# Optimization experiments

Measured on AMD Instinct MI355X. Metric: run time of the kernel, lower is better.

Reference implementation:

```python
import jax, jax.numpy as jnp
import numpy as np

N_STATIONS = 100000
N_TIME = 365
N_NEIGHBORS = 5
SMOOTHING = 0.1


def setup_inputs() -> dict:
    key = jax.random.key(0)
    k = jax.random.split(key, 6)
    N, T, K = N_STATIONS, N_TIME, N_NEIGHBORS
    time_vector = jnp.arange(T, dtype=jnp.float32) / 365.25  # years
    constant_offset = jax.random.normal(k[0], (N,), jnp.float32) * 10.0
    linear_trend = jax.random.normal(k[1], (N,), jnp.float32) * 5.0  # mm/yr (ps00_rates buffer)
    seasonal_amplitudes = jax.random.uniform(k[2], (N, 4), jnp.float32) * 6.0
    seasonal_phases = jax.random.uniform(k[3], (N, 4), jnp.float32) * (2.0 * np.pi)
    neighbor_indices = jax.random.randint(k[4], (N, K), 0, N)
    w = jax.random.uniform(k[5], (N, K), jnp.float32) + 1e-3
    neighbor_weights = w / jnp.sum(w, axis=1, keepdims=True)  # row-normalized, like exp-dist weights
    periods = jnp.array([0.25, 0.5, 1.0, 2.0], dtype=jnp.float32)
    return {
        'time_vector': time_vector,
        'constant_offset': constant_offset,
        'linear_trend': linear_trend,
        'seasonal_amplitudes': seasonal_amplitudes,
        'seasonal_phases': seasonal_phases,
        'neighbor_weights': neighbor_weights,
        'periods': periods,
        'neighbor_indices': neighbor_indices,
    }


def _smooth(p, neighbor_indices, neighbor_weights):
    # p: [N, 4]; vectorized version of per-station loop: gather + weighted mean
    nb = p[neighbor_indices]                                   # [N, K, 4]
    avg = jnp.einsum('nkf,nk->nf', nb, neighbor_weights)       # [N, 4]
    return (1.0 - SMOOTHING) * p + SMOOTHING * avg


def reference(time_vector, constant_offset, linear_trend, seasonal_amplitudes,
              seasonal_phases, neighbor_weights, periods, neighbor_indices):
    amps = _smooth(seasonal_amplitudes, neighbor_indices, neighbor_weights)   # [N, 4]
    phs = _smooth(seasonal_phases, neighbor_indices, neighbor_weights)        # [N, 4]
    t = time_vector[None, :]                                                  # [1, T]
    signals = constant_offset[:, None] + linear_trend[:, None] * t           # [N, T]
    two_pi = jnp.float32(2.0 * np.pi)
    for f in range(4):  # fixed small set of seasonal periods
        freq = 1.0 / periods[f]
        signals = signals + amps[:, f:f + 1] * jnp.sin(two_pi * freq * t + phs[:, f:f + 1])
    return signals
```

## Files before the change

### kernel.cpp

```cpp
#include <hip/hip_runtime.h>
#include <math.h>

typedef float f32x2 __attribute__((ext_vector_type(2)));
typedef float f32x4 __attribute__((ext_vector_type(4)));

#define TWO_PI 6.283185307179586f
#define SMOOTH 0.1f
#define SPW 8
#define WAVES 4
#define BLOCK 256
#define SPB (SPW * WAVES)
#define NPAIR 3

__device__ __forceinline__ f32x2 sp2(float x) { f32x2 r; r.x = x; r.y = x; return r; }
__device__ __forceinline__ float rlane(float v, int l) {
    return __uint_as_float((unsigned)__builtin_amdgcn_readlane((int)__float_as_uint(v), l));
}

template<int TT>
__global__ __launch_bounds__(BLOCK) void fused_v14(
    const float* __restrict__ time_vector,
    const float* __restrict__ constant_offset,
    const float* __restrict__ linear_trend,
    const float* __restrict__ amps,
    const float* __restrict__ phs,
    const float* __restrict__ wgt,
    const float* __restrict__ periods,
    const int*   __restrict__ nbidx,
    float* __restrict__ out,
    int N, int T_rt, int K)
{
    const int T = (TT > 0) ? TT : T_rt;
    extern __shared__ float slab[];

    const int tid    = threadIdx.x;
    const int wave   = tid >> 6;
    const int lane   = tid & 63;
    const int bbase  = blockIdx.x * SPB;
    const int wbase  = bbase + wave * SPW;

    if (bbase >= N) return;
    int bsend = N - bbase; if (bsend > SPB) bsend = SPB;

    int sid = wbase + (lane & (SPW - 1));
    if (sid >= N) sid = N - 1;

    float4 a = reinterpret_cast<const float4*>(amps)[sid];
    float4 p = reinterpret_cast<const float4*>(phs)[sid];

    int   nb[5]; float w[5];
    __builtin_memcpy(nb, nbidx + (size_t)sid * K, 5 * sizeof(int));
    __builtin_memcpy(w,  wgt   + (size_t)sid * K, 5 * sizeof(float));

    float av0 = 0.f, av1 = 0.f, av2 = 0.f, av3 = 0.f;
    float pv0 = 0.f, pv1 = 0.f, pv2 = 0.f, pv3 = 0.f;
    #pragma unroll
    for (int k = 0; k < 5; ++k) {
        float4 na = reinterpret_cast<const float4*>(amps)[nb[k]];
        float4 np = reinterpret_cast<const float4*>(phs)[nb[k]];
        av0 += w[k] * na.x; av1 += w[k] * na.y; av2 += w[k] * na.z; av3 += w[k] * na.w;
        pv0 += w[k] * np.x; pv1 += w[k] * np.y; pv2 += w[k] * np.z; pv3 += w[k] * np.w;
    }
    float sa0 = (1.0f - SMOOTH) * a.x + SMOOTH * av0;
    float sa1 = (1.0f - SMOOTH) * a.y + SMOOTH * av1;
    float sa2 = (1.0f - SMOOTH) * a.z + SMOOTH * av2;
    float sa3 = (1.0f - SMOOTH) * a.w + SMOOTH * av3;
    float sp0 = (1.0f - SMOOTH) * p.x + SMOOTH * pv0;
    float sp1 = (1.0f - SMOOTH) * p.y + SMOOTH * pv1;
    float sp2v = (1.0f - SMOOTH) * p.z + SMOOTH * pv2;
    float sp3 = (1.0f - SMOOTH) * p.w + SMOOTH * pv3;

    float cc = constant_offset[sid];
    float cm = linear_trend[sid];
    float cA0 = sa0 * __cosf(sp0),  cB0 = sa0 * __sinf(sp0);
    float cA1 = sa1 * __cosf(sp1),  cB1 = sa1 * __sinf(sp1);
    float cA2 = sa2 * __cosf(sp2v), cB2 = sa2 * __sinf(sp2v);
    float cA3 = sa3 * __cosf(sp3),  cB3 = sa3 * __sinf(sp3);

    const float w0 = TWO_PI / periods[0];
    const float w1 = TWO_PI / periods[1];
    const float w2 = TWO_PI / periods[2];
    const float w3 = TWO_PI / periods[3];

    f32x2 tv[NPAIR];
    f32x2 bs[NPAIR][4], bc[NPAIR][4];
    bool full[NPAIR], any[NPAIR];
    const int t0 = 2 * lane;

    #pragma unroll
    for (int q = 0; q < NPAIR; ++q) {
        const int t = t0 + 128 * q;
        const bool v0 = (t < T), v1 = (t + 1 < T);
        any[q] = v0; full[q] = v1;
        float ta = v0 ? time_vector[t]     : 0.f;
        float tb = v1 ? time_vector[t + 1] : 0.f;
        f32x2 tvp; tvp.x = ta; tvp.y = tb;
        tv[q] = tvp;
        #pragma unroll
        for (int f = 0; f < 4; ++f) {
            const float wf = (f == 0) ? w0 : (f == 1) ? w1 : (f == 2) ? w2 : w3;
            f32x2 s, c;
            s.x = __sinf(wf * ta); s.y = __sinf(wf * tb);
            c.x = __cosf(wf * ta); c.y = __cosf(wf * tb);
            bs[q][f] = s; bc[q][f] = c;
        }
    }

    if (bsend == SPB) {
        float* wrows = slab + (size_t)(wave * SPW) * T;

        #pragma unroll
        for (int j = 0; j < SPW; ++j) {
            float sc  = rlane(cc,  j), sm  = rlane(cm,  j);
            float sA0 = rlane(cA0, j), sB0 = rlane(cB0, j);
            float sA1 = rlane(cA1, j), sB1 = rlane(cB1, j);
            float sA2 = rlane(cA2, j), sB2 = rlane(cB2, j);
            float sA3 = rlane(cA3, j), sB3 = rlane(cB3, j);
            float* lrow = wrows + j * T;

            #pragma unroll
            for (int q = 0; q < NPAIR; ++q) {
                f32x2 sig = sp2(sc) + sp2(sm) * tv[q];
                sig += sp2(sA0) * bs[q][0] + sp2(sB0) * bc[q][0];
                sig += sp2(sA1) * bs[q][1] + sp2(sB1) * bc[q][1];
                sig += sp2(sA2) * bs[q][2] + sp2(sB2) * bc[q][2];
                sig += sp2(sA3) * bs[q][3] + sp2(sB3) * bc[q][3];
                const int t = t0 + 128 * q;
                if (full[q]) { lrow[t] = sig.x; lrow[t + 1] = sig.y; }
                else if (any[q]) { lrow[t] = sig.x; }
            }
        }

        __syncthreads();

        const f32x4* lsrc = reinterpret_cast<const f32x4*>(slab);
        f32x4* gdst = reinterpret_cast<f32x4*>(out + (size_t)bbase * T);

        if (TT == 365) {
            f32x4 v0_ = lsrc[tid];          f32x4 v1_ = lsrc[tid + 256];
            f32x4 v2_ = lsrc[tid + 512];    f32x4 v3_ = lsrc[tid + 768];
            f32x4 v4_ = lsrc[tid + 1024];   f32x4 v5_ = lsrc[tid + 1280];
            f32x4 v6_ = lsrc[tid + 1536];   f32x4 v7_ = lsrc[tid + 1792];
            f32x4 v8_ = lsrc[tid + 2048];   f32x4 v9_ = lsrc[tid + 2304];
            f32x4 va_ = lsrc[tid + 2560];
            const bool extra = (tid < 104);
            f32x4 vb_;
            if (extra) vb_ = lsrc[tid + 2816];

            __builtin_nontemporal_store(v0_, gdst + tid);
            __builtin_nontemporal_store(v1_, gdst + tid + 256);
            __builtin_nontemporal_store(v2_, gdst + tid + 512);
            __builtin_nontemporal_store(v3_, gdst + tid + 768);
            __builtin_nontemporal_store(v4_, gdst + tid + 1024);
            __builtin_nontemporal_store(v5_, gdst + tid + 1280);
            __builtin_nontemporal_store(v6_, gdst + tid + 1536);
            __builtin_nontemporal_store(v7_, gdst + tid + 1792);
            __builtin_nontemporal_store(v8_, gdst + tid + 2048);
            __builtin_nontemporal_store(v9_, gdst + tid + 2304);
            __builtin_nontemporal_store(va_, gdst + tid + 2560);
            if (extra) __builtin_nontemporal_store(vb_, gdst + tid + 2816);
        } else {
            const int nch = (SPB * T) >> 2;
            for (int i = tid; i < nch; i += BLOCK) {
                f32x4 v = lsrc[i];
                __builtin_nontemporal_store(v, gdst + i);
            }
        }
    } else {
        int send = N - wbase; if (send > SPW) send = SPW;
        if (send <= 0) return;
        float* obase = out + (size_t)wbase * T;
        for (int j = 0; j < send; ++j) {
            float sc  = rlane(cc,  j), sm  = rlane(cm,  j);
            float sA0 = rlane(cA0, j), sB0 = rlane(cB0, j);
            float sA1 = rlane(cA1, j), sB1 = rlane(cB1, j);
            float sA2 = rlane(cA2, j), sB2 = rlane(cB2, j);
            float sA3 = rlane(cA3, j), sB3 = rlane(cB3, j);
            float* orow = obase + (size_t)j * T;
            #pragma unroll
            for (int q = 0; q < NPAIR; ++q) {
                f32x2 sig = sp2(sc) + sp2(sm) * tv[q];
                sig += sp2(sA0) * bs[q][0] + sp2(sB0) * bc[q][0];
                sig += sp2(sA1) * bs[q][1] + sp2(sB1) * bc[q][1];
                sig += sp2(sA2) * bs[q][2] + sp2(sB2) * bc[q][2];
                sig += sp2(sA3) * bs[q][3] + sp2(sB3) * bc[q][3];
                const int t = t0 + 128 * q;
                if (full[q]) { orow[t] = sig.x; orow[t + 1] = sig.y; }
                else if (any[q]) { orow[t] = sig.x; }
            }
        }
    }
}

extern "C" void kernel_launch(void* const* d_in, const int* in_sizes, int n_in,
                              void* d_out, int out_size, void* d_ws, size_t ws_size,
                              hipStream_t stream)
{
    const float* time_vector     = (const float*)d_in[0];
    const float* constant_offset = (const float*)d_in[1];
    const float* linear_trend    = (const float*)d_in[2];
    const float* amps            = (const float*)d_in[3];
    const float* phs             = (const float*)d_in[4];
    const float* wgt             = (const float*)d_in[5];
    const float* periods         = (const float*)d_in[6];
    const int*   nbidx           = (const int*)d_in[7];

    int T = in_sizes[0];
    int N = in_sizes[1];
    int K = in_sizes[5] / N;
    float* out = (float*)d_out;

    int grid = (N + SPB - 1) / SPB;
    size_t shmem = (size_t)SPB * T * sizeof(float);
    if (T == 365) {
        fused_v14<365><<<grid, BLOCK, shmem, stream>>>(
            time_vector, constant_offset, linear_trend, amps, phs, wgt,
            periods, nbidx, out, N, T, K);
    } else {
        fused_v14<0><<<grid, BLOCK, shmem, stream>>>(
            time_vector, constant_offset, linear_trend, amps, phs, wgt,
            periods, nbidx, out, N, T, K);
    }
}
```

Measured before the change: 35.77 us.

## Process four 32-station slabs per block, reusing sin/cos basis and LDS

Each block now handles four consecutive 32-station slabs instead of one. Lanes are split into four groups of eight so that all 32 stations' coefficients for a wave are gathered and smoothed in one pass. The per-thread sin/cos time basis is then reused across the slabs, and a single LDS buffer is recycled with a lightweight lgkmcnt+s_barrier between the compute and store phases. This cuts the grid to a quarter and amortizes the transcendental setup, at the cost of serializing the slabs inside a block and adding two barriers per slab.

```diff
diff --git a/kernel.cpp b/kernel.cpp
--- a/kernel.cpp
+++ b/kernel.cpp
@@ -9,16 +9,20 @@
 #define SPW 8
 #define WAVES 4
 #define BLOCK 256
-#define SPB (SPW * WAVES)
+#define SPB 32
+#define SLABS 4
 #define NPAIR 3
 
 __device__ __forceinline__ f32x2 sp2(float x) { f32x2 r; r.x = x; r.y = x; return r; }
 __device__ __forceinline__ float rlane(float v, int l) {
     return __uint_as_float((unsigned)__builtin_amdgcn_readlane((int)__float_as_uint(v), l));
 }
+__device__ __forceinline__ void barrier_lgkm() {
+    asm volatile("s_waitcnt lgkmcnt(0)\ns_barrier" ::: "memory");
+}
 
 template<int TT>
-__global__ __launch_bounds__(BLOCK) void fused_v14(
+__global__ __launch_bounds__(BLOCK) void fused_v16(
     const float* __restrict__ time_vector,
     const float* __restrict__ constant_offset,
     const float* __restrict__ linear_trend,
@@ -28,21 +32,20 @@
     const float* __restrict__ periods,
     const int*   __restrict__ nbidx,
     float* __restrict__ out,
-    int N, int T_rt, int K)
+    int N, int T_rt, int K, int nslab)
 {
     const int T = (TT > 0) ? TT : T_rt;
     extern __shared__ float slab[];
 
-    const int tid    = threadIdx.x;
-    const int wave   = tid >> 6;
-    const int lane   = tid & 63;
-    const int bbase  = blockIdx.x * SPB;
-    const int wbase  = bbase + wave * SPW;
-
-    if (bbase >= N) return;
-    int bsend = N - bbase; if (bsend > SPB) bsend = SPB;
-
-    int sid = wbase + (lane & (SPW - 1));
+    const int tid   = threadIdx.x;
+    const int wave  = tid >> 6;
+    const int lane  = tid & 63;
+    const int slab0 = blockIdx.x * SLABS;
+    if (slab0 >= nslab) return;
+
+    const int sgrp = (lane >> 3) & (SLABS - 1);
+    const int jrow = lane & 7;
+    int sid = (slab0 + sgrp) * SPB + wave * SPW + jrow;
     if (sid >= N) sid = N - 1;
 
     float4 a = reinterpret_cast<const float4*>(amps)[sid];
@@ -106,87 +109,100 @@
         }
     }
 
-    if (bsend == SPB) {
-        float* wrows = slab + (size_t)(wave * SPW) * T;
-
-        #pragma unroll
-        for (int j = 0; j < SPW; ++j) {
-            float sc  = rlane(cc,  j), sm  = rlane(cm,  j);
-            float sA0 = rlane(cA0, j), sB0 = rlane(cB0, j);
-            float sA1 = rlane(cA1, j), sB1 = rlane(cB1, j);
-            float sA2 = rlane(cA2, j), sB2 = rlane(cB2, j);
-            float sA3 = rlane(cA3, j), sB3 = rlane(cB3, j);
-            float* lrow = wrows + j * T;
-
+    float* wrows = slab + (size_t)(wave * SPW) * T;
+    const f32x4* lsrc = reinterpret_cast<const f32x4*>(slab);
+
+    #pragma unroll
+    for (int s = 0; s < SLABS; ++s) {
+        const int si = slab0 + s;
+        if (si >= nslab) break;
+        const int bbase = si * SPB;
+        const bool fullslab = (bbase + SPB <= N);
+
+        if (fullslab) {
             #pragma unroll
-            for (int q = 0; q < NPAIR; ++q) {
-                f32x2 sig = sp2(sc) + sp2(sm) * tv[q];
-                sig += sp2(sA0) * bs[q][0] + sp2(sB0) * bc[q][0];
-                sig += sp2(sA1) * bs[q][1] + sp2(sB1) * bc[q][1];
-                sig += sp2(sA2) * bs[q][2] + sp2(sB2) * bc[q][2];
-                sig += sp2(sA3) * bs[q][3] + sp2(sB3) * bc[q][3];
-                const int t = t0 + 128 * q;
-                if (full[q]) { lrow[t] = sig.x; lrow[t + 1] = sig.y; }
-                else if (any[q]) { lrow[t] = sig.x; }
+            for (int j = 0; j < SPW; ++j) {
+                const int src = (s << 3) | j;
+                float sc  = rlane(cc,  src), sm  = rlane(cm,  src);
+                float sA0 = rlane(cA0, src), sB0 = rlane(cB0, src);
+                float sA1 = rlane(cA1, src), sB1 = rlane(cB1, src);
+                float sA2 = rlane(cA2, src), sB2 = rlane(cB2, src);
+                float sA3 = rlane(cA3, src), sB3 = rlane(cB3, src);
+                float* lrow = wrows + j * T;
+
+                #pragma unroll
+                for (int q = 0; q < NPAIR; ++q) {
+                    f32x2 sig = sp2(sc) + sp2(sm) * tv[q];
+                    sig += sp2(sA0) * bs[q][0] + sp2(sB0) * bc[q][0];
+                    sig += sp2(sA1) * bs[q][1] + sp2(sB1) * bc[q][1];
+                    sig += sp2(sA2) * bs[q][2] + sp2(sB2) * bc[q][2];
+                    sig += sp2(sA3) * bs[q][3] + sp2(sB3) * bc[q][3];
+                    const int t = t0 + 128 * q;
+                    if (full[q]) { lrow[t] = sig.x; lrow[t + 1] = sig.y; }
+                    else if (any[q]) { lrow[t] = sig.x; }
+                }
             }
-        }
-
-        __syncthreads();
-
-        const f32x4* lsrc = reinterpret_cast<const f32x4*>(slab);
-        f32x4* gdst = reinterpret_cast<f32x4*>(out + (size_t)bbase * T);
-
-        if (TT == 365) {
-            f32x4 v0_ = lsrc[tid];          f32x4 v1_ = lsrc[tid + 256];
-            f32x4 v2_ = lsrc[tid + 512];    f32x4 v3_ = lsrc[tid + 768];
-            f32x4 v4_ = lsrc[tid + 1024];   f32x4 v5_ = lsrc[tid + 1280];
-            f32x4 v6_ = lsrc[tid + 1536];   f32x4 v7_ = lsrc[tid + 1792];
-            f32x4 v8_ = lsrc[tid + 2048];   f32x4 v9_ = lsrc[tid + 2304];
-            f32x4 va_ = lsrc[tid + 2560];
-            const bool extra = (tid < 104);
-            f32x4 vb_;
-            if (extra) vb_ = lsrc[tid + 2816];
-
-            __builtin_nontemporal_store(v0_, gdst + tid);
-            __builtin_nontemporal_store(v1_, gdst + tid + 256);
-            __builtin_nontemporal_store(v2_, gdst + tid + 512);
-            __builtin_nontemporal_store(v3_, gdst + tid + 768);
-            __builtin_nontemporal_store(v4_, gdst + tid + 1024);
-            __builtin_nontemporal_store(v5_, gdst + tid + 1280);
-            __builtin_nontemporal_store(v6_, gdst + tid + 1536);
-            __builtin_nontemporal_store(v7_, gdst + tid + 1792);
-            __builtin_nontemporal_store(v8_, gdst + tid + 2048);
-            __builtin_nontemporal_store(v9_, gdst + tid + 2304);
-            __builtin_nontemporal_store(va_, gdst + tid + 2560);
-            if (extra) __builtin_nontemporal_store(vb_, gdst + tid + 2816);
+
+            barrier_lgkm();
+
+            f32x4* gdst = reinterpret_cast<f32x4*>(out + (size_t)bbase * T);
+            if (TT == 365) {
+                f32x4 v0_ = lsrc[tid];          f32x4 v1_ = lsrc[tid + 256];
+                f32x4 v2_ = lsrc[tid + 512];    f32x4 v3_ = lsrc[tid + 768];
+                f32x4 v4_ = lsrc[tid + 1024];   f32x4 v5_ = lsrc[tid + 1280];
+                f32x4 v6_ = lsrc[tid + 1536];   f32x4 v7_ = lsrc[tid + 1792];
+                f32x4 v8_ = lsrc[tid + 2048];   f32x4 v9_ = lsrc[tid + 2304];
+                f32x4 va_ = lsrc[tid + 2560];
+                const bool extra = (tid < 104);
+                f32x4 vb_;
+                if (extra) vb_ = lsrc[tid + 2816];
+
+                __builtin_nontemporal_store(v0_, gdst + tid);
+                __builtin_nontemporal_store(v1_, gdst + tid + 256);
+                __builtin_nontemporal_store(v2_, gdst + tid + 512);
+                __builtin_nontemporal_store(v3_, gdst + tid + 768);
+                __builtin_nontemporal_store(v4_, gdst + tid + 1024);
+                __builtin_nontemporal_store(v5_, gdst + tid + 1280);
+                __builtin_nontemporal_store(v6_, gdst + tid + 1536);
+                __builtin_nontemporal_store(v7_, gdst + tid + 1792);
+                __builtin_nontemporal_store(v8_, gdst + tid + 2048);
+                __builtin_nontemporal_store(v9_, gdst + tid + 2304);
+                __builtin_nontemporal_store(va_, gdst + tid + 2560);
+                if (extra) __builtin_nontemporal_store(vb_, gdst + tid + 2816);
+            } else {
+                const int nch = (SPB * T) >> 2;
+                for (int i = tid; i < nch; i += BLOCK) {
+                    f32x4 v = lsrc[i];
+                    __builtin_nontemporal_store(v, gdst + i);
+                }
+            }
+
+            barrier_lgkm();
         } else {
-            const int nch = (SPB * T) >> 2;
-            for (int i = tid; i < nch; i += BLOCK) {
-                f32x4 v = lsrc[i];
-                __builtin_nontemporal_store(v, gdst + i);
-            }
-        }
-    } else {
-        int send = N - wbase; if (send > SPW) send = SPW;
-        if (send <= 0) return;
-        float* obase = out + (size_t)wbase * T;
-        for (int j = 0; j < send; ++j) {
-            float sc  = rlane(cc,  j), sm  = rlane(cm,  j);
-            float sA0 = rlane(cA0, j), sB0 = rlane(cB0, j);
-            float sA1 = rlane(cA1, j), sB1 = rlane(cB1, j);
-            float sA2 = rlane(cA2, j), sB2 = rlane(cB2, j);
-            float sA3 = rlane(cA3, j), sB3 = rlane(cB3, j);
-            float* orow = obase + (size_t)j * T;
-            #pragma unroll
-            for (int q = 0; q < NPAIR; ++q) {
-                f32x2 sig = sp2(sc) + sp2(sm) * tv[q];
-                sig += sp2(sA0) * bs[q][0] + sp2(sB0) * bc[q][0];
-                sig += sp2(sA1) * bs[q][1] + sp2(sB1) * bc[q][1];
-                sig += sp2(sA2) * bs[q][2] + sp2(sB2) * bc[q][2];
-                sig += sp2(sA3) * bs[q][3] + sp2(sB3) * bc[q][3];
-                const int t = t0 + 128 * q;
-                if (full[q]) { orow[t] = sig.x; orow[t + 1] = sig.y; }
-                else if (any[q]) { orow[t] = sig.x; }
+            int wfirst = bbase + wave * SPW;
+            int send = N - wfirst; if (send > SPW) send = SPW;
+            if (send > 0) {
+                float* obase = out + (size_t)wfirst * T;
+                for (int j = 0; j < send; ++j) {
+                    const int src = (s << 3) | j;
+                    float sc  = rlane(cc,  src), sm  = rlane(cm,  src);
+                    float sA0 = rlane(cA0, src), sB0 = rlane(cB0, src);
+                    float sA1 = rlane(cA1, src), sB1 = rlane(cB1, src);
+                    float sA2 = rlane(cA2, src), sB2 = rlane(cB2, src);
+                    float sA3 = rlane(cA3, src), sB3 = rlane(cB3, src);
+                    float* orow = obase + (size_t)j * T;
+                    #pragma unroll
+                    for (int q = 0; q < NPAIR; ++q) {
+                        f32x2 sig = sp2(sc) + sp2(sm) * tv[q];
+                        sig += sp2(sA0) * bs[q][0] + sp2(sB0) * bc[q][0];
+                        sig += sp2(sA1) * bs[q][1] + sp2(sB1) * bc[q][1];
+                        sig += sp2(sA2) * bs[q][2] + sp2(sB2) * bc[q][2];
+                        sig += sp2(sA3) * bs[q][3] + sp2(sB3) * bc[q][3];
+                        const int t = t0 + 128 * q;
+                        if (full[q]) { orow[t] = sig.x; orow[t + 1] = sig.y; }
+                        else if (any[q]) { orow[t] = sig.x; }
+                    }
+                }
             }
         }
     }
@@ -210,15 +226,17 @@
     int K = in_sizes[5] / N;
     float* out = (float*)d_out;
 
-    int grid = (N + SPB - 1) / SPB;
+    int nslab = (N + SPB - 1) / SPB;
+    int grid  = (nslab + SLABS - 1) / SLABS;
     size_t shmem = (size_t)SPB * T * sizeof(float);
+
     if (T == 365) {
-        fused_v14<365><<<grid, BLOCK, shmem, stream>>>(
+        fused_v16<365><<<grid, BLOCK, shmem, stream>>>(
             time_vector, constant_offset, linear_trend, amps, phs, wgt,
-            periods, nbidx, out, N, T, K);
+            periods, nbidx, out, N, T, K, nslab);
     } else {
-        fused_v14<0><<<grid, BLOCK, shmem, stream>>>(
+        fused_v16<0><<<grid, BLOCK, shmem, stream>>>(
             time_vector, constant_offset, linear_trend, amps, phs, wgt,
-            periods, nbidx, out, N, T, K);
-    }
-}
+            periods, nbidx, out, N, T, K, nslab);
+    }
+}
```

New measurement: 43.75 us. +22.3%, slower.
